# Kernel optimization log

Measured on AMD Instinct MI355X. Metric: run time of the kernel, lower is better.

## Reference

```python
import jax, jax.numpy as jnp
import numpy as np

def setup_inputs() -> dict:
    key = jax.random.key(0)
    k1, k2, k3 = jax.random.split(key, 3)
    N_net, d, n_t, n_in = 1, 4, 2048, 256
    n_h, n = 8, 256
    STD = 0.02  # E_std / Q_std in the original init
    r_prime = jax.random.normal(k1, (N_net, d, n_t, n_in), dtype=jnp.float32)
    Q = STD * jax.random.normal(k2, (N_net, n_h, n_in, n_in), dtype=jnp.float32)
    E = STD * jax.random.normal(k3, (N_net, n_h, n, n_in), dtype=jnp.float32)
    return {"r_prime": r_prime, "Q": Q, "E": E}

def reference(r_prime, Q, E):
    # r_prime: [N, b, t, i_in]; Q: [N, h, i_in, j_in]; E: [N, h, n, j_in]
    n_t = r_prime.shape[2]
    # Omega[N,b,h,t,u] = r_t^T Q^h r_u  (bilinear attention scores, no softmax)
    Omega = jnp.einsum('Nbti,Nhij,Nbuj->Nbhtu', r_prime, Q, r_prime)
    # Causal mask (lower-triangular Theta), applied inside the second contraction.
    Theta = jnp.tril(jnp.ones((n_t, n_t), dtype=r_prime.dtype))
    # r[N,b,t,i_out] = sum_{u<=t,h} Omega[t,u] * (E^h r_u)_i
    r = jnp.einsum('Nbhtu,tu,Nhij,Nbuj->Nbti', Omega, Theta, E, r_prime)
    return r
```

## Files before the change

kernel.cpp:

```cpp
#include <hip/hip_runtime.h>

typedef __attribute__((ext_vector_type(4))) float f32x4;
typedef __attribute__((ext_vector_type(8))) short s16x8;

#define DEVI static __device__ __forceinline__

constexpr int BB = 4, HH = 8, TT = 2048, DD = 256;

DEVI short f2bf(float f) {
  union { float f; unsigned u; } x; x.f = f;
  unsigned r = x.u + 0x7fffu + ((x.u >> 16) & 1u);
  return (short)(r >> 16);
}

DEVI void gl16(const short* g, short* l) {
  __builtin_amdgcn_global_load_lds(
      (const __attribute__((address_space(1))) void*)g,
      (__attribute__((address_space(3))) void*)l, 16, 0, 0);
}

__global__ void cast_prep(const float* __restrict__ r, const float* __restrict__ Q,
                          const float* __restrict__ E,
                          short* __restrict__ rbf, short* __restrict__ Qt,
                          short* __restrict__ Ebf) {
  int idx = blockIdx.x * blockDim.x + threadIdx.x;
  int stride = gridDim.x * blockDim.x;
  for (int i = idx; i < BB * TT * DD; i += stride) rbf[i] = f2bf(r[i]);
  for (int i = idx; i < HH * DD * DD; i += stride) {
    int h = i / (DD * DD), rem = i % (DD * DD), j = rem / DD, i2 = rem % DD;
    Qt[i] = f2bf(Q[(h * DD + i2) * DD + j]);
    Ebf[i] = f2bf(E[i]);
  }
}

__global__ __launch_bounds__(256, 2)
void prep_gemm(const short* __restrict__ rbf, const short* __restrict__ Qt,
               const short* __restrict__ Ebf, short* __restrict__ Abf,
               short* __restrict__ Vtbf, int mode) {
  __shared__ __align__(16) short w_lds[64 * 256];
  int tid = threadIdx.x, lane = tid & 63, wid = tid >> 6;
  int h = blockIdx.y, b = blockIdx.z, bx = blockIdx.x;
  const short* X; const short* W; short* C; int ldC, m0, n0;
  if (mode == 0) {
    m0 = (bx >> 2) * 64; n0 = (bx & 3) * 64;
    X = rbf + (size_t)b * TT * DD;
    W = Qt + (size_t)h * DD * DD;
    C = Abf + (size_t)(b * HH + h) * TT * DD; ldC = DD;
  } else {
    m0 = (bx & 3) * 64; n0 = (bx >> 2) * 64;
    X = Ebf + (size_t)h * DD * DD;
    W = rbf + (size_t)b * TT * DD;
    C = Vtbf + (size_t)(b * HH + h) * DD * TT; ldC = TT;
  }
  #pragma unroll
  for (int it = 0; it < 8; ++it) {
    int t = it * 256 + tid;
    int row = t >> 5, kb = t & 31;
    s16x8 v = *(const s16x8*)(W + (size_t)(n0 + row) * DD + kb * 8);
    *(s16x8*)(&w_lds[row * 256 + ((kb ^ (row & 7)) << 3)]) = v;
  }
  s16x8 a[8];
  {
    const short* xrow = X + (size_t)(m0 + wid * 16 + (lane & 15)) * DD + (lane >> 4) * 8;
    #pragma unroll
    for (int ks = 0; ks < 8; ++ks) a[ks] = *(const s16x8*)(xrow + ks * 32);
  }
  __syncthreads();
  f32x4 c[4] = {};
  #pragma unroll
  for (int n = 0; n < 4; ++n) {
    int row = n * 16 + (lane & 15);
    #pragma unroll
    for (int ks = 0; ks < 8; ++ks) {
      int kb = ks * 4 + (lane >> 4);
      s16x8 bfr = *(const s16x8*)(&w_lds[row * 256 + ((kb ^ (row & 7)) << 3)]);
      c[n] = __builtin_amdgcn_mfma_f32_16x16x32_bf16(a[ks], bfr, c[n], 0, 0, 0);
    }
  }
  __syncthreads();
  #pragma unroll
  for (int n = 0; n < 4; ++n) {
    int col = n * 16 + (lane & 15);
    int cb = col >> 3;
    #pragma unroll
    for (int rr = 0; rr < 4; ++rr) {
      int row = wid * 16 + (lane >> 4) * 4 + rr;
      w_lds[row * 64 + ((cb ^ (row & 7)) << 3) + (col & 7)] = f2bf(c[n][rr]);
    }
  }
  __syncthreads();
  #pragma unroll
  for (int q = 0; q < 2; ++q) {
    int t = q * 256 + tid;
    int row = t >> 3, cb = t & 7;
    s16x8 v = *(const s16x8*)(&w_lds[row * 64 + ((cb ^ (row & 7)) << 3)]);
    *(s16x8*)(&C[(size_t)(m0 + row) * ldC + n0 + cb * 8]) = v;
  }
}

__global__ __launch_bounds__(256, 1)
void attn_main(const short* __restrict__ Abf, const short* __restrict__ Kbf,
               const short* __restrict__ Vtb, float* __restrict__ out) {
  __shared__ __align__(16) short k_lds[2][64 * 256];
  __shared__ __align__(16) short v_lds[2][256 * 64];
  __shared__ __align__(16) short s_lds[128 * 32];
  int tid = threadIdx.x, lane = tid & 63, wid = tid >> 6;
  int q = blockIdx.x;
  int p = q >> 5, hb = q & 31;
  int h = hb & 7, b = hb >> 3;

  const short* Ab0 = Abf + (size_t)(b * HH + h) * TT * DD;
  const short* Kb = Kbf + (size_t)b * TT * DD;
  const short* Vb = Vtb + (size_t)(b * HH + h) * DD * TT;

#define STAGE(bufi, iu_) do {                                                  \
    int U_ = (iu_) * 64;                                                       \
    const short* ksrc_ = Kb + (size_t)U_ * DD;                                 \
    _Pragma("unroll")                                                          \
    for (int c_ = 0; c_ < 8; ++c_) {                                           \
      int kc_ = wid * 8 + c_;                                                  \
      int row_ = kc_ * 2 + (lane >> 5);                                        \
      int blk_ = lane & 31;                                                    \
      gl16(ksrc_ + (size_t)row_ * DD + ((blk_ ^ (row_ & 7)) << 3),             \
           &k_lds[bufi][kc_ * 512]);                                           \
    }                                                                          \
    _Pragma("unroll")                                                          \
    for (int c_ = 0; c_ < 8; ++c_) {                                           \
      int vc_ = wid * 8 + c_;                                                  \
      int row_ = vc_ * 8 + (lane >> 3);                                        \
      int cb_ = lane & 7;                                                      \
      gl16(Vb + (size_t)row_ * TT + U_ + ((cb_ ^ (row_ & 7)) << 3),            \
           &v_lds[bufi][vc_ * 512]);                                           \
    }                                                                          \
  } while (0)

  #pragma unroll 1
  for (int hv = 0; hv < 2; ++hv) {
    int tt = hv ? (15 - p) : p;
    s16x8 a[2][8];
    {
      const short* abase = Ab0 + (size_t)(tt * 128 + wid * 32 + (lane & 15)) * DD + ((lane >> 4) << 3);
      #pragma unroll
      for (int rb = 0; rb < 2; ++rb)
        #pragma unroll
        for (int ks = 0; ks < 8; ++ks)
          a[rb][ks] = *(const s16x8*)(abase + rb * 16 * DD + ks * 32);
    }
    f32x4 acc[2][16] = {};
    int nU = 2 * tt + 2;

    STAGE(0, 0);

    #pragma unroll 1
    for (int iu = 0; iu < nU; ++iu) {
      int cur = iu & 1;
      if (iu + 1 < nU) {
        STAGE(cur ^ 1, iu + 1);
        asm volatile("s_waitcnt vmcnt(16)" ::: "memory");
      } else {
        asm volatile("s_waitcnt vmcnt(0)" ::: "memory");
      }
      __builtin_amdgcn_s_barrier();
      asm volatile("" ::: "memory");
      int U = iu * 64;

      #pragma unroll
      for (int hh = 0; hh < 2; ++hh) {
        f32x4 s[2][2] = {{{0,0,0,0},{0,0,0,0}},{{0,0,0,0},{0,0,0,0}}};
        #pragma unroll
        for (int n2 = 0; n2 < 2; ++n2) {
          int row = (hh * 2 + n2) * 16 + (lane & 15);
          #pragma unroll
          for (int ks = 0; ks < 8; ++ks) {
            int kb = ks * 4 + (lane >> 4);
            s16x8 bfr = *(const s16x8*)(&k_lds[cur][row * 256 + ((kb ^ (row & 7)) << 3)]);
            s[0][n2] = __builtin_amdgcn_mfma_f32_16x16x32_bf16(a[0][ks], bfr, s[0][n2], 0, 0, 0);
            s[1][n2] = __builtin_amdgcn_mfma_f32_16x16x32_bf16(a[1][ks], bfr, s[1][n2], 0, 0, 0);
          }
        }
        #pragma unroll
        for (int rb = 0; rb < 2; ++rb) {
          #pragma unroll
          for (int n2 = 0; n2 < 2; ++n2) {
            #pragma unroll
            for (int rr = 0; rr < 4; ++rr) {
              int t_loc = wid * 32 + rb * 16 + (lane >> 4) * 4 + rr;
              int u_glob = U + (hh * 2 + n2) * 16 + (lane & 15);
              float v = (u_glob <= tt * 128 + t_loc) ? s[rb][n2][rr] : 0.0f;
              int kloc = n2 * 16 + (lane & 15);
              int cb = kloc >> 3;
              s_lds[t_loc * 32 + ((cb ^ ((t_loc >> 1) & 3)) << 3) + (kloc & 7)] = f2bf(v);
            }
          }
        }
        s16x8 af[2];
        #pragma unroll
        for (int rb = 0; rb < 2; ++rb) {
          int R = wid * 32 + rb * 16 + (lane & 15);
          int cb2 = (lane >> 4) ^ ((R >> 1) & 3);
          af[rb] = *(const s16x8*)(&s_lds[R * 32 + (cb2 << 3)]);
        }
        #pragma unroll
        for (int ni = 0; ni < 16; ++ni) {
          int vrow = ni * 16 + (lane & 15);
          int ub = hh * 4 + (lane >> 4);
          s16x8 bv = *(const s16x8*)(&v_lds[cur][vrow * 64 + ((ub ^ (vrow & 7)) << 3)]);
          acc[0][ni] = __builtin_amdgcn_mfma_f32_16x16x32_bf16(af[0], bv, acc[0][ni], 0, 0, 0);
          acc[1][ni] = __builtin_amdgcn_mfma_f32_16x16x32_bf16(af[1], bv, acc[1][ni], 0, 0, 0);
        }
      }
      asm volatile("s_waitcnt lgkmcnt(0)" ::: "memory");
      __builtin_amdgcn_s_barrier();
    }

    float* ob = out + ((size_t)b * TT + tt * 128 + wid * 32) * DD;
    #pragma unroll
    for (int rb = 0; rb < 2; ++rb) {
      #pragma unroll
      for (int ni = 0; ni < 16; ++ni) {
        int col = ni * 16 + (lane & 15);
        #pragma unroll
        for (int rr = 0; rr < 4; ++rr) {
          int row = rb * 16 + (lane >> 4) * 4 + rr;
          atomicAdd(&ob[row * DD + col], acc[rb][ni][rr]);
        }
      }
    }
  }
#undef STAGE
}

extern "C" void kernel_launch(void* const* d_in, const int* in_sizes, int n_in,
                              void* d_out, int out_size, void* d_ws, size_t ws_size,
                              hipStream_t stream) {
  const float* r = (const float*)d_in[0];
  const float* Q = (const float*)d_in[1];
  const float* E = (const float*)d_in[2];
  float* out = (float*)d_out;
  char* ws = (char*)d_ws;

  size_t off = 0;
  short* rbf = (short*)(ws + off); off += (size_t)BB * TT * DD * 2;
  short* Qt  = (short*)(ws + off); off += (size_t)HH * DD * DD * 2;
  short* Ebf = (short*)(ws + off); off += (size_t)HH * DD * DD * 2;
  short* Abf = (short*)(ws + off); off += (size_t)BB * HH * TT * DD * 2;
  short* Vtb = (short*)(ws + off); off += (size_t)BB * HH * DD * TT * 2;

  hipMemsetAsync(d_out, 0, (size_t)out_size * sizeof(float), stream);
  cast_prep<<<1024, 256, 0, stream>>>(r, Q, E, rbf, Qt, Ebf);
  prep_gemm<<<dim3(128, HH, BB), 256, 0, stream>>>(rbf, Qt, Ebf, Abf, Vtb, 0);
  prep_gemm<<<dim3(128, HH, BB), 256, 0, stream>>>(rbf, Qt, Ebf, Abf, Vtb, 1);
  attn_main<<<dim3(256, 1, 1), 256, 0, stream>>>(Abf, rbf, Vtb, out);
}
```

Measured before the change: 229.0 us.

## Vectorize casts, tile Q transpose, merge prep GEMMs, read V directly from global

The cast kernel now converts r and E with vector loads and stores, and Q's transpose moves to a separate LDS-tiled kernel so its reads are coalesced. The two prep GEMM launches become one launch, with the mode taken from blockIdx. The attention kernel no longer stages V in LDS and loads the V fragments straight from global memory, which halves LDS use and raises the launch bound to two blocks per CU. The cost is strided, uncached-in-LDS global reads of V inside the inner MFMA loop, which may stall on memory latency.

New measurement: 873.7 us. +281.5%, slower.

```diff
diff --git a/kernel.cpp b/kernel.cpp
--- a/kernel.cpp
+++ b/kernel.cpp
@@ -19,27 +19,62 @@
       (__attribute__((address_space(3))) void*)l, 16, 0, 0);
 }
 
-__global__ void cast_prep(const float* __restrict__ r, const float* __restrict__ Q,
-                          const float* __restrict__ E,
-                          short* __restrict__ rbf, short* __restrict__ Qt,
-                          short* __restrict__ Ebf) {
+__global__ void cast_rE(const float* __restrict__ r, const float* __restrict__ E,
+                        short* __restrict__ rbf, short* __restrict__ Ebf) {
   int idx = blockIdx.x * blockDim.x + threadIdx.x;
   int stride = gridDim.x * blockDim.x;
-  for (int i = idx; i < BB * TT * DD; i += stride) rbf[i] = f2bf(r[i]);
-  for (int i = idx; i < HH * DD * DD; i += stride) {
-    int h = i / (DD * DD), rem = i % (DD * DD), j = rem / DD, i2 = rem % DD;
-    Qt[i] = f2bf(Q[(h * DD + i2) * DD + j]);
-    Ebf[i] = f2bf(E[i]);
+  int nR = BB * TT * DD / 8, nE = HH * DD * DD / 8;
+  for (int i = idx; i < nR; i += stride) {
+    f32x4 x0 = ((const f32x4*)r)[2 * i], x1 = ((const f32x4*)r)[2 * i + 1];
+    s16x8 o;
+    #pragma unroll
+    for (int e = 0; e < 4; ++e) { o[e] = f2bf(x0[e]); o[4 + e] = f2bf(x1[e]); }
+    ((s16x8*)rbf)[i] = o;
+  }
+  for (int i = idx; i < nE; i += stride) {
+    f32x4 x0 = ((const f32x4*)E)[2 * i], x1 = ((const f32x4*)E)[2 * i + 1];
+    s16x8 o;
+    #pragma unroll
+    for (int e = 0; e < 4; ++e) { o[e] = f2bf(x0[e]); o[4 + e] = f2bf(x1[e]); }
+    ((s16x8*)Ebf)[i] = o;
+  }
+}
+
+__global__ void qt_prep(const float* __restrict__ Q, short* __restrict__ Qt) {
+  __shared__ float t[64][65];
+  int tid = threadIdx.x;
+  int h = blockIdx.y, bx = blockIdx.x;
+  int i0 = (bx >> 2) * 64, j0 = (bx & 3) * 64;
+  const float* Qh = Q + (size_t)h * DD * DD;
+  int rr = tid >> 2, cq = tid & 3;
+  #pragma unroll
+  for (int it = 0; it < 4; ++it) {
+    int col = cq * 16 + it * 4;
+    f32x4 v = *(const f32x4*)(Qh + (size_t)(i0 + rr) * DD + j0 + col);
+    #pragma unroll
+    for (int e = 0; e < 4; ++e) t[rr][col + e] = v[e];
+  }
+  __syncthreads();
+  int j = tid >> 2, iq = tid & 3;
+  short* dst = Qt + (size_t)h * DD * DD + (size_t)(j0 + j) * DD + i0;
+  #pragma unroll
+  for (int it = 0; it < 4; ++it) {
+    int ic = iq * 16 + it * 4;
+    short o[4];
+    #pragma unroll
+    for (int e = 0; e < 4; ++e) o[e] = f2bf(t[ic + e][j]);
+    *(int2*)(dst + ic) = *(int2*)o;
   }
 }
 
 __global__ __launch_bounds__(256, 2)
 void prep_gemm(const short* __restrict__ rbf, const short* __restrict__ Qt,
                const short* __restrict__ Ebf, short* __restrict__ Abf,
-               short* __restrict__ Vtbf, int mode) {
+               short* __restrict__ Vtbf) {
   __shared__ __align__(16) short w_lds[64 * 256];
   int tid = threadIdx.x, lane = tid & 63, wid = tid >> 6;
-  int h = blockIdx.y, b = blockIdx.z, bx = blockIdx.x;
+  int h = blockIdx.y, b = blockIdx.z;
+  int mode = blockIdx.x >> 7, bx = blockIdx.x & 127;
   const short* X; const short* W; short* C; int ldC, m0, n0;
   if (mode == 0) {
     m0 = (bx >> 2) * 64; n0 = (bx & 3) * 64;
@@ -98,11 +133,10 @@
   }
 }
 
-__global__ __launch_bounds__(256, 1)
+__global__ __launch_bounds__(256, 2)
 void attn_main(const short* __restrict__ Abf, const short* __restrict__ Kbf,
                const short* __restrict__ Vtb, float* __restrict__ out) {
   __shared__ __align__(16) short k_lds[2][64 * 256];
-  __shared__ __align__(16) short v_lds[2][256 * 64];
   __shared__ __align__(16) short s_lds[128 * 32];
   int tid = threadIdx.x, lane = tid & 63, wid = tid >> 6;
   int q = blockIdx.x;
@@ -124,14 +158,6 @@
       gl16(ksrc_ + (size_t)row_ * DD + ((blk_ ^ (row_ & 7)) << 3),             \
            &k_lds[bufi][kc_ * 512]);                                           \
     }                                                                          \
-    _Pragma("unroll")                                                          \
-    for (int c_ = 0; c_ < 8; ++c_) {                                           \
-      int vc_ = wid * 8 + c_;                                                  \
-      int row_ = vc_ * 8 + (lane >> 3);                                        \
-      int cb_ = lane & 7;                                                      \
-      gl16(Vb + (size_t)row_ * TT + U_ + ((cb_ ^ (row_ & 7)) << 3),            \
-           &v_lds[bufi][vc_ * 512]);                                           \
-    }                                                                          \
   } while (0)
 
   #pragma unroll 1
@@ -156,12 +182,11 @@
       int cur = iu & 1;
       if (iu + 1 < nU) {
         STAGE(cur ^ 1, iu + 1);
-        asm volatile("s_waitcnt vmcnt(16)" ::: "memory");
+        asm volatile("s_waitcnt vmcnt(8)" ::: "memory");
       } else {
         asm volatile("s_waitcnt vmcnt(0)" ::: "memory");
       }
       __builtin_amdgcn_s_barrier();
-      asm volatile("" ::: "memory");
       int U = iu * 64;
 
       #pragma unroll
@@ -200,11 +225,10 @@
           int cb2 = (lane >> 4) ^ ((R >> 1) & 3);
           af[rb] = *(const s16x8*)(&s_lds[R * 32 + (cb2 << 3)]);
         }
+        const short* vb2 = Vb + (size_t)(lane & 15) * TT + U + hh * 32 + ((lane >> 4) << 3);
         #pragma unroll
         for (int ni = 0; ni < 16; ++ni) {
-          int vrow = ni * 16 + (lane & 15);
-          int ub = hh * 4 + (lane >> 4);
-          s16x8 bv = *(const s16x8*)(&v_lds[cur][vrow * 64 + ((ub ^ (vrow & 7)) << 3)]);
+          s16x8 bv = *(const s16x8*)(vb2 + (size_t)ni * (16 * TT));
           acc[0][ni] = __builtin_amdgcn_mfma_f32_16x16x32_bf16(af[0], bv, acc[0][ni], 0, 0, 0);
           acc[1][ni] = __builtin_amdgcn_mfma_f32_16x16x32_bf16(af[1], bv, acc[1][ni], 0, 0, 0);
         }
@@ -247,8 +271,8 @@
   short* Vtb = (short*)(ws + off); off += (size_t)BB * HH * DD * TT * 2;
 
   hipMemsetAsync(d_out, 0, (size_t)out_size * sizeof(float), stream);
-  cast_prep<<<1024, 256, 0, stream>>>(r, Q, E, rbf, Qt, Ebf);
-  prep_gemm<<<dim3(128, HH, BB), 256, 0, stream>>>(rbf, Qt, Ebf, Abf, Vtb, 0);
-  prep_gemm<<<dim3(128, HH, BB), 256, 0, stream>>>(rbf, Qt, Ebf, Abf, Vtb, 1);
+  cast_rE<<<1024, 256, 0, stream>>>(r, E, rbf, Ebf);
+  qt_prep<<<dim3(16, HH), 256, 0, stream>>>(Q, Qt);
+  prep_gemm<<<dim3(256, HH, BB), 256, 0, stream>>>(rbf, Qt, Ebf, Abf, Vtb);
   attn_main<<<dim3(256, 1, 1), 256, 0, stream>>>(Abf, rbf, Vtb, out);
 }
```
